# Performance work log

Hardware: AMD Instinct MI355X
Metric: run time of the kernel (lower is better)

Reference implementation:

```python
import jax, jax.numpy as jnp
import numpy as np

COND = 128  # mask = first 128 dims are condition (True); last 128 are transformed


def _mlp(h, W1, b1, W2, b2, W3, b3):
    h = jax.nn.relu(h @ W1 + b1)
    h = jax.nn.relu(h @ W2 + b2)
    return h @ W3 + b3


def setup_inputs() -> dict:
    key = jax.random.key(0)
    ks = jax.random.split(key, 8)
    B, D, H, T = 65536, 256, 512, 128
    s = 0.02  # small init so exp(tanh(s_vals)) is well-behaved
    inp = {
        "x": jax.random.normal(ks[0], (B, D), dtype=jnp.float32),
        "Ws1": jax.random.normal(ks[1], (COND, H), dtype=jnp.float32) * s,
        "bs1": jnp.zeros((H,), jnp.float32),
        "Ws2": jax.random.normal(ks[2], (H, H), dtype=jnp.float32) * s,
        "bs2": jnp.zeros((H,), jnp.float32),
        "Ws3": jax.random.normal(ks[3], (H, T), dtype=jnp.float32) * s,
        "bs3": jnp.zeros((T,), jnp.float32),
        "Wt1": jax.random.normal(ks[4], (COND, H), dtype=jnp.float32) * s,
        "bt1": jnp.zeros((H,), jnp.float32),
        "Wt2": jax.random.normal(ks[5], (H, H), dtype=jnp.float32) * s,
        "bt2": jnp.zeros((H,), jnp.float32),
        "Wt3": jax.random.normal(ks[6], (H, T), dtype=jnp.float32) * s,
        "bt3": jnp.zeros((T,), jnp.float32),
    }
    return inp


def reference(x, Ws1, bs1, Ws2, bs2, Ws3, bs3, Wt1, bt1, Wt2, bt2, Wt3, bt3):
    # mask gather: condition = masked dims, transform = the rest
    cond = x[:, :COND]            # [B, COND]
    x_t = x[:, COND:]             # [B, T]
    s_vals = jnp.tanh(_mlp(cond, Ws1, bs1, Ws2, bs2, Ws3, bs3))  # [B, T]
    t_vals = _mlp(cond, Wt1, bt1, Wt2, bt2, Wt3, bt3)            # [B, T]
    y_partial = x_t * jnp.exp(s_vals) + t_vals                   # forward branch (inverse=False)
    log_det = s_vals.sum(axis=1)                                 # [B]
    y = jnp.concatenate([cond, y_partial], axis=1)               # scatter back
    return (y, log_det)
```

## Files before the change

kernel.cpp:

```cpp
#include <hip/hip_runtime.h>
#include <hip/hip_bf16.h>

typedef __bf16          bf16x8_t __attribute__((ext_vector_type(8)));
typedef float           f32x4_t  __attribute__((ext_vector_type(4)));
typedef unsigned short  u16x4_t  __attribute__((ext_vector_type(4)));

#define DIN      256
#define CONDN    128
#define BM       64
#define NTHREADS 512
#define NWAVE    8

#define OFF_WS1 0
#define OFF_WS2 65536
#define OFF_WS3 327680
#define OFF_WT1 393216
#define OFF_WT2 458752
#define OFF_WT3 720896
#define W_TOTAL 786432

__global__ void prep_w(const float* __restrict__ Ws1, const float* __restrict__ Ws2,
                       const float* __restrict__ Ws3, const float* __restrict__ Wt1,
                       const float* __restrict__ Wt2, const float* __restrict__ Wt3,
                       __hip_bfloat16* __restrict__ wt) {
  int idx = blockIdx.x * blockDim.x + threadIdx.x;
  if (idx >= W_TOTAL) return;
  const float* W; int K, N, off;
  if (idx < OFF_WS2)      { W = Ws1; K = 128; N = 512; off = idx - OFF_WS1; }
  else if (idx < OFF_WS3) { W = Ws2; K = 512; N = 512; off = idx - OFF_WS2; }
  else if (idx < OFF_WT1) { W = Ws3; K = 512; N = 128; off = idx - OFF_WS3; }
  else if (idx < OFF_WT2) { W = Wt1; K = 128; N = 512; off = idx - OFF_WT1; }
  else if (idx < OFF_WT3) { W = Wt2; K = 512; N = 512; off = idx - OFF_WT2; }
  else                    { W = Wt3; K = 512; N = 128; off = idx - OFF_WT3; }
  int n = off / K;
  int k = off - n * K;
  wt[idx] = __float2bfloat16(W[k * N + n]);
}

#define SWZ(row, col) (((((col) >> 3) ^ ((row) & 7)) << 3) + ((col) & 7))

template<int KTOT, int MT, int NT>
__device__ __forceinline__ void mm_tile(const __hip_bfloat16* __restrict__ As, const int lda,
                                        const __hip_bfloat16* __restrict__ Bsrc,
                                        const int l15, const int l4, f32x4_t acc[MT][NT]) {
  const int xr = l15 & 7;
  bf16x8_t a[MT], b[NT], bn[NT];
  #pragma unroll
  for (int n = 0; n < NT; ++n)
    b[n] = *reinterpret_cast<const bf16x8_t*>(&Bsrc[(n * 16 + l15) * KTOT + l4 * 8]);
  #pragma unroll
  for (int kk = 0; kk < KTOT; kk += 32) {
    if (kk + 32 < KTOT) {
      #pragma unroll
      for (int n = 0; n < NT; ++n)
        bn[n] = *reinterpret_cast<const bf16x8_t*>(&Bsrc[(n * 16 + l15) * KTOT + kk + 32 + l4 * 8]);
    }
    #pragma unroll
    for (int m = 0; m < MT; ++m)
      a[m] = *reinterpret_cast<const bf16x8_t*>(
          &As[(m * 16 + l15) * lda + ((((kk >> 3) + l4) ^ xr) << 3)]);
    #pragma unroll
    for (int m = 0; m < MT; ++m) {
      #pragma unroll
      for (int n = 0; n < NT; ++n)
        acc[m][n] = __builtin_amdgcn_mfma_f32_16x16x32_bf16(a[m], b[n], acc[m][n], 0, 0, 0);
    }
    if (kk + 32 < KTOT) {
      #pragma unroll
      for (int n = 0; n < NT; ++n) b[n] = bn[n];
    }
  }
}

template<int MT, int NT, int LD>
__device__ __forceinline__ void relu_store(f32x4_t acc[MT][NT], const float* __restrict__ bias,
                                           const int n0, const int l15, const int l4,
                                           __hip_bfloat16* __restrict__ H) {
  #pragma unroll
  for (int n = 0; n < NT; ++n) {
    const int col = n0 + n * 16 + l15;
    const float bv = bias[col];
    #pragma unroll
    for (int m = 0; m < MT; ++m) {
      #pragma unroll
      for (int r = 0; r < 4; ++r) {
        const int row = m * 16 + l4 * 4 + r;
        float v = fmaxf(acc[m][n][r] + bv, 0.0f);
        H[row * LD + SWZ(row, col)] = __float2bfloat16(v);
      }
    }
  }
}

#define ZERO_ACC(acc, MT, NT) do {                       \
    _Pragma("unroll") for (int m_ = 0; m_ < MT; ++m_)    \
    _Pragma("unroll") for (int n_ = 0; n_ < NT; ++n_)    \
      acc[m_][n_] = (f32x4_t){0.f, 0.f, 0.f, 0.f};       \
  } while (0)

__global__ __launch_bounds__(NTHREADS, 2)
void realnvp_fused(const float* __restrict__ x, const __hip_bfloat16* __restrict__ wt,
                   const float* __restrict__ bs1, const float* __restrict__ bs2,
                   const float* __restrict__ bs3, const float* __restrict__ bt1,
                   const float* __restrict__ bt2, const float* __restrict__ bt3,
                   float* __restrict__ y, float* __restrict__ ld) {
  __shared__ __hip_bfloat16 sA[BM * CONDN];
  __shared__ __hip_bfloat16 sH[BM * 512];
  float* sLd = reinterpret_cast<float*>(sA);

  const int tid  = threadIdx.x;
  const int lane = tid & 63;
  const int wid  = tid >> 6;
  const int l15  = lane & 15;
  const int l4   = lane >> 4;
  const int row0 = blockIdx.x * BM;
  const int n0   = wid * 64;
  const int n3   = wid * 16;

  #pragma unroll
  for (int i = 0; i < 4; ++i) {
    int f = tid + i * NTHREADS;
    int r = f >> 5;
    int c = (f & 31) << 2;
    const float4 v = *reinterpret_cast<const float4*>(&x[(size_t)(row0 + r) * DIN + c]);
    *reinterpret_cast<float4*>(&y[(size_t)(row0 + r) * DIN + c]) = v;
    union { u16x4_t u; __hip_bfloat16 b[4]; } p;
    p.b[0] = __float2bfloat16(v.x); p.b[1] = __float2bfloat16(v.y);
    p.b[2] = __float2bfloat16(v.z); p.b[3] = __float2bfloat16(v.w);
    *reinterpret_cast<u16x4_t*>(&sA[r * CONDN + SWZ(r, c)]) = p.u;
  }
  __syncthreads();

  f32x4_t acc[4][4];
  f32x4_t sfrag[4], tfrag[4];

  ZERO_ACC(acc, 4, 4);
  mm_tile<128, 4, 4>(sA, CONDN, wt + OFF_WS1 + (size_t)n0 * 128, l15, l4, acc);
  relu_store<4, 4, 512>(acc, bs1, n0, l15, l4, sH);
  __syncthreads();
  ZERO_ACC(acc, 4, 4);
  mm_tile<512, 4, 4>(sH, 512, wt + OFF_WS2 + (size_t)n0 * 512, l15, l4, acc);
  __syncthreads();
  relu_store<4, 4, 512>(acc, bs2, n0, l15, l4, sH);
  __syncthreads();
  {
    f32x4_t a3[4][1];
    ZERO_ACC(a3, 4, 1);
    mm_tile<512, 4, 1>(sH, 512, wt + OFF_WS3 + (size_t)n3 * 512, l15, l4, a3);
    #pragma unroll
    for (int m = 0; m < 4; ++m) sfrag[m] = a3[m][0];
  }
  __syncthreads();

  ZERO_ACC(acc, 4, 4);
  mm_tile<128, 4, 4>(sA, CONDN, wt + OFF_WT1 + (size_t)n0 * 128, l15, l4, acc);
  relu_store<4, 4, 512>(acc, bt1, n0, l15, l4, sH);
  __syncthreads();
  ZERO_ACC(acc, 4, 4);
  mm_tile<512, 4, 4>(sH, 512, wt + OFF_WT2 + (size_t)n0 * 512, l15, l4, acc);
  __syncthreads();
  relu_store<4, 4, 512>(acc, bt2, n0, l15, l4, sH);
  __syncthreads();
  {
    f32x4_t a3[4][1];
    ZERO_ACC(a3, 4, 1);
    mm_tile<512, 4, 1>(sH, 512, wt + OFF_WT3 + (size_t)n3 * 512, l15, l4, a3);
    #pragma unroll
    for (int m = 0; m < 4; ++m) tfrag[m] = a3[m][0];
  }

  const float bsv = bs3[n3 + l15];
  const float btv = bt3[n3 + l15];
  #pragma unroll
  for (int m = 0; m < 4; ++m) {
    #pragma unroll
    for (int r = 0; r < 4; ++r) {
      const int rl   = m * 16 + l4 * 4 + r;
      const int grow = row0 + rl;
      const int col  = n3 + l15;
      float s = tanhf(sfrag[m][r] + bsv);
      float t = tfrag[m][r] + btv;
      float xv = x[(size_t)grow * DIN + CONDN + col];
      y[(size_t)grow * DIN + CONDN + col] = xv * expf(s) + t;
      float ss = s;
      ss += __shfl_xor(ss, 1);
      ss += __shfl_xor(ss, 2);
      ss += __shfl_xor(ss, 4);
      ss += __shfl_xor(ss, 8);
      if (l15 == 0) sLd[wid * BM + rl] = ss;
    }
  }
  __syncthreads();
  if (tid < BM) {
    float v = 0.f;
    #pragma unroll
    for (int w = 0; w < NWAVE; ++w) v += sLd[w * BM + tid];
    ld[row0 + tid] = v;
  }
}

extern "C" void kernel_launch(void* const* d_in, const int* in_sizes, int n_in,
                              void* d_out, int out_size, void* d_ws, size_t ws_size,
                              hipStream_t stream) {
  const float* x   = (const float*)d_in[0];
  const float* Ws1 = (const float*)d_in[1];
  const float* bs1 = (const float*)d_in[2];
  const float* Ws2 = (const float*)d_in[3];
  const float* bs2 = (const float*)d_in[4];
  const float* Ws3 = (const float*)d_in[5];
  const float* bs3 = (const float*)d_in[6];
  const float* Wt1 = (const float*)d_in[7];
  const float* bt1 = (const float*)d_in[8];
  const float* Wt2 = (const float*)d_in[9];
  const float* bt2 = (const float*)d_in[10];
  const float* Wt3 = (const float*)d_in[11];
  const float* bt3 = (const float*)d_in[12];

  const int Btot = in_sizes[0] / DIN;
  float* y  = (float*)d_out;
  float* ld = (float*)d_out + (size_t)Btot * DIN;
  __hip_bfloat16* wt = (__hip_bfloat16*)d_ws;

  prep_w<<<(W_TOTAL + 255) / 256, 256, 0, stream>>>(Ws1, Ws2, Ws3, Wt1, Wt2, Wt3, wt);
  realnvp_fused<<<Btot / BM, NTHREADS, 0, stream>>>(x, wt, bs1, bs2, bs3,
                                                    bt1, bt2, bt3, y, ld);
}
```

Measured before the change: 240.4 us.

## Enlarge row tile to 112 rows and add ring-buffered N=1 output GEMM

The per-block row tile grows from 64 to 112 rows (7 MFMA m-tiles per wave), with bounds handling for a ragged last block. Each weight fragment loaded from global/L2 is now reused across more rows. Occupancy drops to one block per SM, since launch bounds and the larger LDS footprint allow only one. A dedicated final-layer GEMM keeps a 4-deep ring of prefetched weight fragments, and the main k-loop is only partially unrolled to limit register pressure.

```diff
diff --git a/kernel.cpp b/kernel.cpp
--- a/kernel.cpp
+++ b/kernel.cpp
@@ -7,7 +7,8 @@
 
 #define DIN      256
 #define CONDN    128
-#define BM       64
+#define BM       112
+#define MT       7
 #define NTHREADS 512
 #define NWAVE    8
 
@@ -39,28 +40,29 @@
 
 #define SWZ(row, col) (((((col) >> 3) ^ ((row) & 7)) << 3) + ((col) & 7))
 
-template<int KTOT, int MT, int NT>
+template<int KTOT, int MTT, int NT>
 __device__ __forceinline__ void mm_tile(const __hip_bfloat16* __restrict__ As, const int lda,
                                         const __hip_bfloat16* __restrict__ Bsrc,
-                                        const int l15, const int l4, f32x4_t acc[MT][NT]) {
+                                        const int l15, const int l4, f32x4_t acc[MTT][NT]) {
   const int xr = l15 & 7;
-  bf16x8_t a[MT], b[NT], bn[NT];
+  const __hip_bfloat16* bp = Bsrc + (size_t)l15 * KTOT + l4 * 8;
+  bf16x8_t a[MTT], b[NT], bn[NT];
   #pragma unroll
   for (int n = 0; n < NT; ++n)
-    b[n] = *reinterpret_cast<const bf16x8_t*>(&Bsrc[(n * 16 + l15) * KTOT + l4 * 8]);
-  #pragma unroll
+    b[n] = *reinterpret_cast<const bf16x8_t*>(bp + n * 16 * KTOT);
+  #pragma unroll 4
   for (int kk = 0; kk < KTOT; kk += 32) {
     if (kk + 32 < KTOT) {
       #pragma unroll
       for (int n = 0; n < NT; ++n)
-        bn[n] = *reinterpret_cast<const bf16x8_t*>(&Bsrc[(n * 16 + l15) * KTOT + kk + 32 + l4 * 8]);
-    }
-    #pragma unroll
-    for (int m = 0; m < MT; ++m)
+        bn[n] = *reinterpret_cast<const bf16x8_t*>(bp + n * 16 * KTOT + kk + 32);
+    }
+    #pragma unroll
+    for (int m = 0; m < MTT; ++m)
       a[m] = *reinterpret_cast<const bf16x8_t*>(
           &As[(m * 16 + l15) * lda + ((((kk >> 3) + l4) ^ xr) << 3)]);
     #pragma unroll
-    for (int m = 0; m < MT; ++m) {
+    for (int m = 0; m < MTT; ++m) {
       #pragma unroll
       for (int n = 0; n < NT; ++n)
         acc[m][n] = __builtin_amdgcn_mfma_f32_16x16x32_bf16(a[m], b[n], acc[m][n], 0, 0, 0);
@@ -72,8 +74,33 @@
   }
 }
 
-template<int MT, int NT, int LD>
-__device__ __forceinline__ void relu_store(f32x4_t acc[MT][NT], const float* __restrict__ bias,
+template<int KTOT, int MTT>
+__device__ __forceinline__ void mm_tile_n1(const __hip_bfloat16* __restrict__ As, const int lda,
+                                           const __hip_bfloat16* __restrict__ Bsrc,
+                                           const int l15, const int l4, f32x4_t acc[MTT]) {
+  const int xr = l15 & 7;
+  const __hip_bfloat16* bp = Bsrc + (size_t)l15 * KTOT + l4 * 8;
+  constexpr int NS = KTOT / 32;
+  bf16x8_t ring[4], a[MTT];
+  #pragma unroll
+  for (int p = 0; p < 4 && p < NS; ++p)
+    ring[p] = *reinterpret_cast<const bf16x8_t*>(bp + p * 32);
+  #pragma unroll
+  for (int s = 0; s < NS; ++s) {
+    #pragma unroll
+    for (int m = 0; m < MTT; ++m)
+      a[m] = *reinterpret_cast<const bf16x8_t*>(
+          &As[(m * 16 + l15) * lda + (((s * 4 + l4) ^ xr) << 3)]);
+    #pragma unroll
+    for (int m = 0; m < MTT; ++m)
+      acc[m] = __builtin_amdgcn_mfma_f32_16x16x32_bf16(a[m], ring[s & 3], acc[m], 0, 0, 0);
+    if (s + 4 < NS)
+      ring[s & 3] = *reinterpret_cast<const bf16x8_t*>(bp + (s + 4) * 32);
+  }
+}
+
+template<int MTT, int NT, int LD>
+__device__ __forceinline__ void relu_store(f32x4_t acc[MTT][NT], const float* __restrict__ bias,
                                            const int n0, const int l15, const int l4,
                                            __hip_bfloat16* __restrict__ H) {
   #pragma unroll
@@ -81,7 +108,7 @@
     const int col = n0 + n * 16 + l15;
     const float bv = bias[col];
     #pragma unroll
-    for (int m = 0; m < MT; ++m) {
+    for (int m = 0; m < MTT; ++m) {
       #pragma unroll
       for (int r = 0; r < 4; ++r) {
         const int row = m * 16 + l4 * 4 + r;
@@ -92,18 +119,18 @@
   }
 }
 
-#define ZERO_ACC(acc, MT, NT) do {                       \
-    _Pragma("unroll") for (int m_ = 0; m_ < MT; ++m_)    \
-    _Pragma("unroll") for (int n_ = 0; n_ < NT; ++n_)    \
-      acc[m_][n_] = (f32x4_t){0.f, 0.f, 0.f, 0.f};       \
+#define ZERO_ACC(acc, MTT, NT) do {                       \
+    _Pragma("unroll") for (int m_ = 0; m_ < MTT; ++m_)    \
+    _Pragma("unroll") for (int n_ = 0; n_ < NT; ++n_)     \
+      acc[m_][n_] = (f32x4_t){0.f, 0.f, 0.f, 0.f};        \
   } while (0)
 
-__global__ __launch_bounds__(NTHREADS, 2)
+__global__ __launch_bounds__(NTHREADS, 1)
 void realnvp_fused(const float* __restrict__ x, const __hip_bfloat16* __restrict__ wt,
                    const float* __restrict__ bs1, const float* __restrict__ bs2,
                    const float* __restrict__ bs3, const float* __restrict__ bt1,
                    const float* __restrict__ bt2, const float* __restrict__ bt3,
-                   float* __restrict__ y, float* __restrict__ ld) {
+                   float* __restrict__ y, float* __restrict__ ld, const int Btot) {
   __shared__ __hip_bfloat16 sA[BM * CONDN];
   __shared__ __hip_bfloat16 sH[BM * 512];
   float* sLd = reinterpret_cast<float*>(sA);
@@ -114,74 +141,83 @@
   const int l15  = lane & 15;
   const int l4   = lane >> 4;
   const int row0 = blockIdx.x * BM;
+  const int V    = min(BM, Btot - row0);
   const int n0   = wid * 64;
   const int n3   = wid * 16;
 
   #pragma unroll
-  for (int i = 0; i < 4; ++i) {
+  for (int i = 0; i < 7; ++i) {
     int f = tid + i * NTHREADS;
     int r = f >> 5;
     int c = (f & 31) << 2;
-    const float4 v = *reinterpret_cast<const float4*>(&x[(size_t)(row0 + r) * DIN + c]);
-    *reinterpret_cast<float4*>(&y[(size_t)(row0 + r) * DIN + c]) = v;
-    union { u16x4_t u; __hip_bfloat16 b[4]; } p;
-    p.b[0] = __float2bfloat16(v.x); p.b[1] = __float2bfloat16(v.y);
-    p.b[2] = __float2bfloat16(v.z); p.b[3] = __float2bfloat16(v.w);
-    *reinterpret_cast<u16x4_t*>(&sA[r * CONDN + SWZ(r, c)]) = p.u;
-  }
-  __syncthreads();
-
-  f32x4_t acc[4][4];
-  f32x4_t sfrag[4], tfrag[4];
-
-  ZERO_ACC(acc, 4, 4);
-  mm_tile<128, 4, 4>(sA, CONDN, wt + OFF_WS1 + (size_t)n0 * 128, l15, l4, acc);
-  relu_store<4, 4, 512>(acc, bs1, n0, l15, l4, sH);
-  __syncthreads();
-  ZERO_ACC(acc, 4, 4);
-  mm_tile<512, 4, 4>(sH, 512, wt + OFF_WS2 + (size_t)n0 * 512, l15, l4, acc);
-  __syncthreads();
-  relu_store<4, 4, 512>(acc, bs2, n0, l15, l4, sH);
+    if (r < V) {
+      const float4 v = *reinterpret_cast<const float4*>(&x[(size_t)(row0 + r) * DIN + c]);
+      *reinterpret_cast<float4*>(&y[(size_t)(row0 + r) * DIN + c]) = v;
+      union { u16x4_t u; __hip_bfloat16 b[4]; } p;
+      p.b[0] = __float2bfloat16(v.x); p.b[1] = __float2bfloat16(v.y);
+      p.b[2] = __float2bfloat16(v.z); p.b[3] = __float2bfloat16(v.w);
+      *reinterpret_cast<u16x4_t*>(&sA[r * CONDN + SWZ(r, c)]) = p.u;
+    } else {
+      *reinterpret_cast<u16x4_t*>(&sA[r * CONDN + SWZ(r, c)]) = (u16x4_t){0, 0, 0, 0};
+    }
+  }
+  __syncthreads();
+
+  f32x4_t acc[MT][4];
+  f32x4_t sfrag[MT], tfrag[MT];
+
+  ZERO_ACC(acc, MT, 4);
+  mm_tile<128, MT, 4>(sA, CONDN, wt + OFF_WS1 + (size_t)n0 * 128, l15, l4, acc);
+  relu_store<MT, 4, 512>(acc, bs1, n0, l15, l4, sH);
+  __syncthreads();
+  ZERO_ACC(acc, MT, 4);
+  mm_tile<512, MT, 4>(sH, 512, wt + OFF_WS2 + (size_t)n0 * 512, l15, l4, acc);
+  __syncthreads();
+  relu_store<MT, 4, 512>(acc, bs2, n0, l15, l4, sH);
   __syncthreads();
   {
-    f32x4_t a3[4][1];
-    ZERO_ACC(a3, 4, 1);
-    mm_tile<512, 4, 1>(sH, 512, wt + OFF_WS3 + (size_t)n3 * 512, l15, l4, a3);
-    #pragma unroll
-    for (int m = 0; m < 4; ++m) sfrag[m] = a3[m][0];
-  }
-  __syncthreads();
-
-  ZERO_ACC(acc, 4, 4);
-  mm_tile<128, 4, 4>(sA, CONDN, wt + OFF_WT1 + (size_t)n0 * 128, l15, l4, acc);
-  relu_store<4, 4, 512>(acc, bt1, n0, l15, l4, sH);
-  __syncthreads();
-  ZERO_ACC(acc, 4, 4);
-  mm_tile<512, 4, 4>(sH, 512, wt + OFF_WT2 + (size_t)n0 * 512, l15, l4, acc);
-  __syncthreads();
-  relu_store<4, 4, 512>(acc, bt2, n0, l15, l4, sH);
+    f32x4_t a3[MT];
+    #pragma unroll
+    for (int m = 0; m < MT; ++m) a3[m] = (f32x4_t){0.f, 0.f, 0.f, 0.f};
+    mm_tile_n1<512, MT>(sH, 512, wt + OFF_WS3 + (size_t)n3 * 512, l15, l4, a3);
+    #pragma unroll
+    for (int m = 0; m < MT; ++m) sfrag[m] = a3[m];
+  }
+  __syncthreads();
+
+  ZERO_ACC(acc, MT, 4);
+  mm_tile<128, MT, 4>(sA, CONDN, wt + OFF_WT1 + (size_t)n0 * 128, l15, l4, acc);
+  relu_store<MT, 4, 512>(acc, bt1, n0, l15, l4, sH);
+  __syncthreads();
+  ZERO_ACC(acc, MT, 4);
+  mm_tile<512, MT, 4>(sH, 512, wt + OFF_WT2 + (size_t)n0 * 512, l15, l4, acc);
+  __syncthreads();
+  relu_store<MT, 4, 512>(acc, bt2, n0, l15, l4, sH);
   __syncthreads();
   {
-    f32x4_t a3[4][1];
-    ZERO_ACC(a3, 4, 1);
-    mm_tile<512, 4, 1>(sH, 512, wt + OFF_WT3 + (size_t)n3 * 512, l15, l4, a3);
-    #pragma unroll
-    for (int m = 0; m < 4; ++m) tfrag[m] = a3[m][0];
+    f32x4_t a3[MT];
+    #pragma unroll
+    for (int m = 0; m < MT; ++m) a3[m] = (f32x4_t){0.f, 0.f, 0.f, 0.f};
+    mm_tile_n1<512, MT>(sH, 512, wt + OFF_WT3 + (size_t)n3 * 512, l15, l4, a3);
+    #pragma unroll
+    for (int m = 0; m < MT; ++m) tfrag[m] = a3[m];
   }
 
   const float bsv = bs3[n3 + l15];
   const float btv = bt3[n3 + l15];
   #pragma unroll
-  for (int m = 0; m < 4; ++m) {
+  for (int m = 0; m < MT; ++m) {
     #pragma unroll
     for (int r = 0; r < 4; ++r) {
       const int rl   = m * 16 + l4 * 4 + r;
       const int grow = row0 + rl;
       const int col  = n3 + l15;
       float s = tanhf(sfrag[m][r] + bsv);
-      float t = tfrag[m][r] + btv;
-      float xv = x[(size_t)grow * DIN + CONDN + col];
-      y[(size_t)grow * DIN + CONDN + col] = xv * expf(s) + t;
+      if (grow < Btot) {
+        float t  = tfrag[m][r] + btv;
+        float xv = x[(size_t)grow * DIN + CONDN + col];
+        y[(size_t)grow * DIN + CONDN + col] = xv * expf(s) + t;
+      }
       float ss = s;
       ss += __shfl_xor(ss, 1);
       ss += __shfl_xor(ss, 2);
@@ -191,7 +227,7 @@
     }
   }
   __syncthreads();
-  if (tid < BM) {
+  if (tid < BM && row0 + tid < Btot) {
     float v = 0.f;
     #pragma unroll
     for (int w = 0; w < NWAVE; ++w) v += sLd[w * BM + tid];
@@ -222,6 +258,7 @@
   __hip_bfloat16* wt = (__hip_bfloat16*)d_ws;
 
   prep_w<<<(W_TOTAL + 255) / 256, 256, 0, stream>>>(Ws1, Ws2, Ws3, Wt1, Wt2, Wt3, wt);
-  realnvp_fused<<<Btot / BM, NTHREADS, 0, stream>>>(x, wt, bs1, bs2, bs3,
-                                                    bt1, bt2, bt3, y, ld);
-}
+  const int grid = (Btot + BM - 1) / BM;
+  realnvp_fused<<<grid, NTHREADS, 0, stream>>>(x, wt, bs1, bs2, bs3,
+                                               bt1, bt2, bt3, y, ld, Btot);
+}
```

Result: slower. 431.3 us (+79.4%).

## Use 16 waves per block with split-K final layer and deeper B prefetch ring

Applied to the files above, without the earlier changes.

Doubles the block to 1024 threads (16 waves), so each wave computes 32 hidden columns instead of 64. The final 512→128 layers are split along K across two wave groups, with partial sums combined through new LDS buffers. The B-operand register prefetch becomes a 3-deep ring. The aim is more latency hiding and less per-wave register pressure, at the cost of more LDS, an extra barrier, occupancy limited to one block per CU, and half the waves idling in the epilogue.

```diff
diff --git a/kernel.cpp b/kernel.cpp
--- a/kernel.cpp
+++ b/kernel.cpp
@@ -8,8 +8,9 @@
 #define DIN      256
 #define CONDN    128
 #define BM       64
-#define NTHREADS 512
-#define NWAVE    8
+#define NTHREADS 1024
+#define NWAVE    16
+#define LDS_S    132
 
 #define OFF_WS1 0
 #define OFF_WS2 65536
@@ -39,41 +40,44 @@
 
 #define SWZ(row, col) (((((col) >> 3) ^ ((row) & 7)) << 3) + ((col) & 7))
 
-template<int KTOT, int MT, int NT>
+template<int KTOT, int LDB, int MTT, int NT>
 __device__ __forceinline__ void mm_tile(const __hip_bfloat16* __restrict__ As, const int lda,
                                         const __hip_bfloat16* __restrict__ Bsrc,
-                                        const int l15, const int l4, f32x4_t acc[MT][NT]) {
+                                        const int l15, const int l4, f32x4_t acc[MTT][NT]) {
   const int xr = l15 & 7;
-  bf16x8_t a[MT], b[NT], bn[NT];
-  #pragma unroll
-  for (int n = 0; n < NT; ++n)
-    b[n] = *reinterpret_cast<const bf16x8_t*>(&Bsrc[(n * 16 + l15) * KTOT + l4 * 8]);
-  #pragma unroll
-  for (int kk = 0; kk < KTOT; kk += 32) {
-    if (kk + 32 < KTOT) {
+  const __hip_bfloat16* bp = Bsrc + (size_t)l15 * LDB + l4 * 8;
+  constexpr int NS = KTOT / 32;
+  constexpr int DEPTH = (NS < 3) ? NS : 3;
+  bf16x8_t ring[DEPTH][NT];
+  bf16x8_t a[MTT];
+  #pragma unroll
+  for (int p = 0; p < DEPTH; ++p) {
+    #pragma unroll
+    for (int n = 0; n < NT; ++n)
+      ring[p][n] = *reinterpret_cast<const bf16x8_t*>(bp + (size_t)n * 16 * LDB + p * 32);
+  }
+  #pragma unroll
+  for (int s = 0; s < NS; ++s) {
+    #pragma unroll
+    for (int m = 0; m < MTT; ++m)
+      a[m] = *reinterpret_cast<const bf16x8_t*>(
+          &As[(m * 16 + l15) * lda + (((s * 4 + l4) ^ xr) << 3)]);
+    #pragma unroll
+    for (int m = 0; m < MTT; ++m) {
       #pragma unroll
       for (int n = 0; n < NT; ++n)
-        bn[n] = *reinterpret_cast<const bf16x8_t*>(&Bsrc[(n * 16 + l15) * KTOT + kk + 32 + l4 * 8]);
-    }
-    #pragma unroll
-    for (int m = 0; m < MT; ++m)
-      a[m] = *reinterpret_cast<const bf16x8_t*>(
-          &As[(m * 16 + l15) * lda + ((((kk >> 3) + l4) ^ xr) << 3)]);
-    #pragma unroll
-    for (int m = 0; m < MT; ++m) {
+        acc[m][n] = __builtin_amdgcn_mfma_f32_16x16x32_bf16(a[m], ring[s % DEPTH][n], acc[m][n], 0, 0, 0);
+    }
+    if (s + DEPTH < NS) {
       #pragma unroll
       for (int n = 0; n < NT; ++n)
-        acc[m][n] = __builtin_amdgcn_mfma_f32_16x16x32_bf16(a[m], b[n], acc[m][n], 0, 0, 0);
-    }
-    if (kk + 32 < KTOT) {
-      #pragma unroll
-      for (int n = 0; n < NT; ++n) b[n] = bn[n];
-    }
-  }
-}
-
-template<int MT, int NT, int LD>
-__device__ __forceinline__ void relu_store(f32x4_t acc[MT][NT], const float* __restrict__ bias,
+        ring[s % DEPTH][n] = *reinterpret_cast<const bf16x8_t*>(bp + (size_t)n * 16 * LDB + (s + DEPTH) * 32);
+    }
+  }
+}
+
+template<int MTT, int NT, int LD>
+__device__ __forceinline__ void relu_store(f32x4_t acc[MTT][NT], const float* __restrict__ bias,
                                            const int n0, const int l15, const int l4,
                                            __hip_bfloat16* __restrict__ H) {
   #pragma unroll
@@ -81,7 +85,7 @@
     const int col = n0 + n * 16 + l15;
     const float bv = bias[col];
     #pragma unroll
-    for (int m = 0; m < MT; ++m) {
+    for (int m = 0; m < MTT; ++m) {
       #pragma unroll
       for (int r = 0; r < 4; ++r) {
         const int row = m * 16 + l4 * 4 + r;
@@ -92,13 +96,13 @@
   }
 }
 
-#define ZERO_ACC(acc, MT, NT) do {                       \
-    _Pragma("unroll") for (int m_ = 0; m_ < MT; ++m_)    \
-    _Pragma("unroll") for (int n_ = 0; n_ < NT; ++n_)    \
-      acc[m_][n_] = (f32x4_t){0.f, 0.f, 0.f, 0.f};       \
+#define ZERO_ACC(acc, MTT, NT) do {                       \
+    _Pragma("unroll") for (int m_ = 0; m_ < MTT; ++m_)    \
+    _Pragma("unroll") for (int n_ = 0; n_ < NT; ++n_)     \
+      acc[m_][n_] = (f32x4_t){0.f, 0.f, 0.f, 0.f};        \
   } while (0)
 
-__global__ __launch_bounds__(NTHREADS, 2)
+__global__ __launch_bounds__(NTHREADS, 1)
 void realnvp_fused(const float* __restrict__ x, const __hip_bfloat16* __restrict__ wt,
                    const float* __restrict__ bs1, const float* __restrict__ bs2,
                    const float* __restrict__ bs3, const float* __restrict__ bt1,
@@ -106,6 +110,8 @@
                    float* __restrict__ y, float* __restrict__ ld) {
   __shared__ __hip_bfloat16 sA[BM * CONDN];
   __shared__ __hip_bfloat16 sH[BM * 512];
+  __shared__ float sS[BM * LDS_S];
+  __shared__ float tS[BM * LDS_S];
   float* sLd = reinterpret_cast<float*>(sA);
 
   const int tid  = threadIdx.x;
@@ -114,11 +120,13 @@
   const int l15  = lane & 15;
   const int l4   = lane >> 4;
   const int row0 = blockIdx.x * BM;
-  const int n0   = wid * 64;
-  const int n3   = wid * 16;
-
-  #pragma unroll
-  for (int i = 0; i < 4; ++i) {
+  const int n0   = wid * 32;
+  const int g    = wid >> 3;
+  const int wA   = wid & 7;
+  const int n3   = wA * 16;
+
+  #pragma unroll
+  for (int i = 0; i < 2; ++i) {
     int f = tid + i * NTHREADS;
     int r = f >> 5;
     int c = (f & 31) << 2;
@@ -131,70 +139,91 @@
   }
   __syncthreads();
 
-  f32x4_t acc[4][4];
+  f32x4_t acc[4][2];
   f32x4_t sfrag[4], tfrag[4];
 
-  ZERO_ACC(acc, 4, 4);
-  mm_tile<128, 4, 4>(sA, CONDN, wt + OFF_WS1 + (size_t)n0 * 128, l15, l4, acc);
-  relu_store<4, 4, 512>(acc, bs1, n0, l15, l4, sH);
-  __syncthreads();
-  ZERO_ACC(acc, 4, 4);
-  mm_tile<512, 4, 4>(sH, 512, wt + OFF_WS2 + (size_t)n0 * 512, l15, l4, acc);
-  __syncthreads();
-  relu_store<4, 4, 512>(acc, bs2, n0, l15, l4, sH);
+  ZERO_ACC(acc, 4, 2);
+  mm_tile<128, 128, 4, 2>(sA, CONDN, wt + OFF_WS1 + (size_t)n0 * 128, l15, l4, acc);
+  relu_store<4, 2, 512>(acc, bs1, n0, l15, l4, sH);
+  __syncthreads();
+  ZERO_ACC(acc, 4, 2);
+  mm_tile<512, 512, 4, 2>(sH, 512, wt + OFF_WS2 + (size_t)n0 * 512, l15, l4, acc);
+  __syncthreads();
+  relu_store<4, 2, 512>(acc, bs2, n0, l15, l4, sH);
   __syncthreads();
   {
     f32x4_t a3[4][1];
     ZERO_ACC(a3, 4, 1);
-    mm_tile<512, 4, 1>(sH, 512, wt + OFF_WS3 + (size_t)n3 * 512, l15, l4, a3);
-    #pragma unroll
-    for (int m = 0; m < 4; ++m) sfrag[m] = a3[m][0];
-  }
-  __syncthreads();
-
-  ZERO_ACC(acc, 4, 4);
-  mm_tile<128, 4, 4>(sA, CONDN, wt + OFF_WT1 + (size_t)n0 * 128, l15, l4, acc);
-  relu_store<4, 4, 512>(acc, bt1, n0, l15, l4, sH);
-  __syncthreads();
-  ZERO_ACC(acc, 4, 4);
-  mm_tile<512, 4, 4>(sH, 512, wt + OFF_WT2 + (size_t)n0 * 512, l15, l4, acc);
-  __syncthreads();
-  relu_store<4, 4, 512>(acc, bt2, n0, l15, l4, sH);
+    mm_tile<256, 512, 4, 1>(sH + g * 256, 512,
+                            wt + OFF_WS3 + (size_t)n3 * 512 + g * 256, l15, l4, a3);
+    if (g == 0) {
+      #pragma unroll
+      for (int m = 0; m < 4; ++m) sfrag[m] = a3[m][0];
+    } else {
+      #pragma unroll
+      for (int m = 0; m < 4; ++m)
+        #pragma unroll
+        for (int r = 0; r < 4; ++r)
+          sS[(m * 16 + l4 * 4 + r) * LDS_S + n3 + l15] = a3[m][0][r];
+    }
+  }
+  __syncthreads();
+
+  ZERO_ACC(acc, 4, 2);
+  mm_tile<128, 128, 4, 2>(sA, CONDN, wt + OFF_WT1 + (size_t)n0 * 128, l15, l4, acc);
+  relu_store<4, 2, 512>(acc, bt1, n0, l15, l4, sH);
+  __syncthreads();
+  ZERO_ACC(acc, 4, 2);
+  mm_tile<512, 512, 4, 2>(sH, 512, wt + OFF_WT2 + (size_t)n0 * 512, l15, l4, acc);
+  __syncthreads();
+  relu_store<4, 2, 512>(acc, bt2, n0, l15, l4, sH);
   __syncthreads();
   {
     f32x4_t a3[4][1];
     ZERO_ACC(a3, 4, 1);
-    mm_tile<512, 4, 1>(sH, 512, wt + OFF_WT3 + (size_t)n3 * 512, l15, l4, a3);
-    #pragma unroll
-    for (int m = 0; m < 4; ++m) tfrag[m] = a3[m][0];
-  }
-
-  const float bsv = bs3[n3 + l15];
-  const float btv = bt3[n3 + l15];
-  #pragma unroll
-  for (int m = 0; m < 4; ++m) {
-    #pragma unroll
-    for (int r = 0; r < 4; ++r) {
-      const int rl   = m * 16 + l4 * 4 + r;
-      const int grow = row0 + rl;
-      const int col  = n3 + l15;
-      float s = tanhf(sfrag[m][r] + bsv);
-      float t = tfrag[m][r] + btv;
-      float xv = x[(size_t)grow * DIN + CONDN + col];
-      y[(size_t)grow * DIN + CONDN + col] = xv * expf(s) + t;
-      float ss = s;
-      ss += __shfl_xor(ss, 1);
-      ss += __shfl_xor(ss, 2);
-      ss += __shfl_xor(ss, 4);
-      ss += __shfl_xor(ss, 8);
-      if (l15 == 0) sLd[wid * BM + rl] = ss;
+    mm_tile<256, 512, 4, 1>(sH + g * 256, 512,
+                            wt + OFF_WT3 + (size_t)n3 * 512 + g * 256, l15, l4, a3);
+    if (g == 0) {
+      #pragma unroll
+      for (int m = 0; m < 4; ++m) tfrag[m] = a3[m][0];
+    } else {
+      #pragma unroll
+      for (int m = 0; m < 4; ++m)
+        #pragma unroll
+        for (int r = 0; r < 4; ++r)
+          tS[(m * 16 + l4 * 4 + r) * LDS_S + n3 + l15] = a3[m][0][r];
+    }
+  }
+  __syncthreads();
+
+  if (g == 0) {
+    const float bsv = bs3[n3 + l15];
+    const float btv = bt3[n3 + l15];
+    #pragma unroll
+    for (int m = 0; m < 4; ++m) {
+      #pragma unroll
+      for (int r = 0; r < 4; ++r) {
+        const int rl   = m * 16 + l4 * 4 + r;
+        const int grow = row0 + rl;
+        const int col  = n3 + l15;
+        float s = tanhf(sfrag[m][r] + sS[rl * LDS_S + col] + bsv);
+        float t = tfrag[m][r] + tS[rl * LDS_S + col] + btv;
+        float xv = x[(size_t)grow * DIN + CONDN + col];
+        y[(size_t)grow * DIN + CONDN + col] = xv * expf(s) + t;
+        float ss = s;
+        ss += __shfl_xor(ss, 1);
+        ss += __shfl_xor(ss, 2);
+        ss += __shfl_xor(ss, 4);
+        ss += __shfl_xor(ss, 8);
+        if (l15 == 0) sLd[wA * BM + rl] = ss;
+      }
     }
   }
   __syncthreads();
   if (tid < BM) {
     float v = 0.f;
     #pragma unroll
-    for (int w = 0; w < NWAVE; ++w) v += sLd[w * BM + tid];
+    for (int w = 0; w < 8; ++w) v += sLd[w * BM + tid];
     ld[row0 + tid] = v;
   }
 }
```

Measured after the change: 271.8 us. 1.13x slower.

## Stage weight tiles into LDS with double-buffered async global_load_lds pipeline

Applied to the files above, without the earlier changes.

Re-layouts the bf16 weights into 32-wide K tiles and streams each tile into a double-buffered LDS region with global_load_lds, prefetching the next tile (including the next layer's first tile) while MFMAs run on the current one. Each wave now reads its B fragments from LDS instead of from global memory, so the whole block shares one fetch of each weight tile. The cost is an extra 64KB of LDS and a block barrier per K step. Launch bounds drop to one block per SM-pair setting, which lowers occupancy.

```diff
diff --git a/kernel.cpp b/kernel.cpp
--- a/kernel.cpp
+++ b/kernel.cpp
@@ -10,6 +10,7 @@
 #define BM       64
 #define NTHREADS 512
 #define NWAVE    8
+#define BUFE     16384
 
 #define OFF_WS1 0
 #define OFF_WS2 65536
@@ -25,55 +26,87 @@
                        __hip_bfloat16* __restrict__ wt) {
   int idx = blockIdx.x * blockDim.x + threadIdx.x;
   if (idx >= W_TOTAL) return;
-  const float* W; int K, N, off;
-  if (idx < OFF_WS2)      { W = Ws1; K = 128; N = 512; off = idx - OFF_WS1; }
-  else if (idx < OFF_WS3) { W = Ws2; K = 512; N = 512; off = idx - OFF_WS2; }
-  else if (idx < OFF_WT1) { W = Ws3; K = 512; N = 128; off = idx - OFF_WS3; }
-  else if (idx < OFF_WT2) { W = Wt1; K = 128; N = 512; off = idx - OFF_WT1; }
-  else if (idx < OFF_WT3) { W = Wt2; K = 512; N = 512; off = idx - OFF_WT2; }
-  else                    { W = Wt3; K = 512; N = 128; off = idx - OFF_WT3; }
-  int n = off / K;
-  int k = off - n * K;
-  wt[idx] = __float2bfloat16(W[k * N + n]);
+  const float* W; int lgN, off;
+  if (idx < OFF_WS2)      { W = Ws1; lgN = 9; off = OFF_WS1; }
+  else if (idx < OFF_WS3) { W = Ws2; lgN = 9; off = OFF_WS2; }
+  else if (idx < OFF_WT1) { W = Ws3; lgN = 7; off = OFF_WS3; }
+  else if (idx < OFF_WT2) { W = Wt1; lgN = 9; off = OFF_WT1; }
+  else if (idx < OFF_WT3) { W = Wt2; lgN = 9; off = OFF_WT2; }
+  else                    { W = Wt3; lgN = 7; off = OFF_WT3; }
+  const int e    = idx - off;
+  const int lgT  = lgN + 5;
+  const int tile = e >> lgT;
+  const int rem  = e & ((1 << lgT) - 1);
+  const int c    = rem >> 3;
+  const int j    = rem & 7;
+  const int o    = c >> lgN;
+  const int n    = c & ((1 << lgN) - 1);
+  const int k    = tile * 32 + o * 8 + j;
+  wt[idx] = __float2bfloat16(W[(k << lgN) + n]);
 }
 
 #define SWZ(row, col) (((((col) >> 3) ^ ((row) & 7)) << 3) + ((col) & 7))
 
-template<int KTOT, int MT, int NT>
-__device__ __forceinline__ void mm_tile(const __hip_bfloat16* __restrict__ As, const int lda,
-                                        const __hip_bfloat16* __restrict__ Bsrc,
-                                        const int l15, const int l4, f32x4_t acc[MT][NT]) {
+template<int NTILE>
+__device__ __forceinline__ void stage_w(__hip_bfloat16* __restrict__ dstbuf,
+                                        const __hip_bfloat16* __restrict__ src0,
+                                        const int wid, const int lane) {
+  constexpr int ROUNDS = (NTILE * 4) / 512;
+  #pragma unroll
+  for (int r = 0; r < ROUNDS; ++r) {
+    const int cbase = (r * 8 + wid) * 64;
+    const __hip_bfloat16* src = src0 + (size_t)(cbase + lane) * 8;
+    __hip_bfloat16* dst = dstbuf + (size_t)cbase * 8;
+    __builtin_amdgcn_global_load_lds(
+        (const __attribute__((address_space(1))) void*)src,
+        (__attribute__((address_space(3))) void*)dst, 16, 0, 0);
+  }
+}
+
+template<int NS, int NTILE, int MTT, int NT, class NextFn>
+__device__ __forceinline__ void gemm_layer(
+    const __hip_bfloat16* __restrict__ As, const int lda,
+    const __hip_bfloat16* __restrict__ wseg, __hip_bfloat16* __restrict__ sW,
+    unsigned& tc, const int wid, const int lane, const int l15, const int l4,
+    const int n0, f32x4_t acc[MTT][NT], NextFn next_stage)
+{
   const int xr = l15 & 7;
-  bf16x8_t a[MT], b[NT], bn[NT];
-  #pragma unroll
-  for (int n = 0; n < NT; ++n)
-    b[n] = *reinterpret_cast<const bf16x8_t*>(&Bsrc[(n * 16 + l15) * KTOT + l4 * 8]);
-  #pragma unroll
-  for (int kk = 0; kk < KTOT; kk += 32) {
-    if (kk + 32 < KTOT) {
-      #pragma unroll
-      for (int n = 0; n < NT; ++n)
-        bn[n] = *reinterpret_cast<const bf16x8_t*>(&Bsrc[(n * 16 + l15) * KTOT + kk + 32 + l4 * 8]);
-    }
-    #pragma unroll
-    for (int m = 0; m < MT; ++m)
-      a[m] = *reinterpret_cast<const bf16x8_t*>(
-          &As[(m * 16 + l15) * lda + ((((kk >> 3) + l4) ^ xr) << 3)]);
-    #pragma unroll
-    for (int m = 0; m < MT; ++m) {
+  bf16x8_t a[MTT], an[MTT], b[NT];
+  #pragma unroll
+  for (int m = 0; m < MTT; ++m)
+    a[m] = *reinterpret_cast<const bf16x8_t*>(&As[(m * 16 + l15) * lda + ((l4 ^ xr) << 3)]);
+  #pragma unroll 1
+  for (int s = 0; s < NS; ++s) {
+    __hip_bfloat16* nbuf = sW + ((tc + 1) & 1) * BUFE;
+    if (s + 1 < NS) stage_w<NTILE>(nbuf, wseg + (size_t)(s + 1) * (NTILE * 32), wid, lane);
+    else            next_stage(nbuf);
+    const __hip_bfloat16* cbuf = sW + (tc & 1) * BUFE;
+    #pragma unroll
+    for (int n = 0; n < NT; ++n)
+      b[n] = *reinterpret_cast<const bf16x8_t*>(&cbuf[(size_t)(l4 * NTILE + n0 + n * 16 + l15) * 8]);
+    if (s + 1 < NS) {
+      #pragma unroll
+      for (int m = 0; m < MTT; ++m)
+        an[m] = *reinterpret_cast<const bf16x8_t*>(
+            &As[(m * 16 + l15) * lda + ((((s + 1) * 4 + l4) ^ xr) << 3)]);
+    }
+    #pragma unroll
+    for (int m = 0; m < MTT; ++m) {
       #pragma unroll
       for (int n = 0; n < NT; ++n)
         acc[m][n] = __builtin_amdgcn_mfma_f32_16x16x32_bf16(a[m], b[n], acc[m][n], 0, 0, 0);
     }
-    if (kk + 32 < KTOT) {
-      #pragma unroll
-      for (int n = 0; n < NT; ++n) b[n] = bn[n];
-    }
-  }
-}
-
-template<int MT, int NT, int LD>
-__device__ __forceinline__ void relu_store(f32x4_t acc[MT][NT], const float* __restrict__ bias,
+    if (s + 1 < NS) {
+      #pragma unroll
+      for (int m = 0; m < MTT; ++m) a[m] = an[m];
+    }
+    ++tc;
+    __syncthreads();
+  }
+}
+
+template<int MTT, int NT, int LD>
+__device__ __forceinline__ void relu_store(f32x4_t acc[MTT][NT], const float* __restrict__ bias,
                                            const int n0, const int l15, const int l4,
                                            __hip_bfloat16* __restrict__ H) {
   #pragma unroll
@@ -81,7 +114,7 @@
     const int col = n0 + n * 16 + l15;
     const float bv = bias[col];
     #pragma unroll
-    for (int m = 0; m < MT; ++m) {
+    for (int m = 0; m < MTT; ++m) {
       #pragma unroll
       for (int r = 0; r < 4; ++r) {
         const int row = m * 16 + l4 * 4 + r;
@@ -92,13 +125,13 @@
   }
 }
 
-#define ZERO_ACC(acc, MT, NT) do {                       \
-    _Pragma("unroll") for (int m_ = 0; m_ < MT; ++m_)    \
-    _Pragma("unroll") for (int n_ = 0; n_ < NT; ++n_)    \
-      acc[m_][n_] = (f32x4_t){0.f, 0.f, 0.f, 0.f};       \
+#define ZERO_ACC(acc, MTT, NT) do {                       \
+    _Pragma("unroll") for (int m_ = 0; m_ < MTT; ++m_)    \
+    _Pragma("unroll") for (int n_ = 0; n_ < NT; ++n_)     \
+      acc[m_][n_] = (f32x4_t){0.f, 0.f, 0.f, 0.f};        \
   } while (0)
 
-__global__ __launch_bounds__(NTHREADS, 2)
+__global__ __launch_bounds__(NTHREADS, 1)
 void realnvp_fused(const float* __restrict__ x, const __hip_bfloat16* __restrict__ wt,
                    const float* __restrict__ bs1, const float* __restrict__ bs2,
                    const float* __restrict__ bs3, const float* __restrict__ bt1,
@@ -106,6 +139,7 @@
                    float* __restrict__ y, float* __restrict__ ld) {
   __shared__ __hip_bfloat16 sA[BM * CONDN];
   __shared__ __hip_bfloat16 sH[BM * 512];
+  __shared__ __hip_bfloat16 sW[2 * BUFE];
   float* sLd = reinterpret_cast<float*>(sA);
 
   const int tid  = threadIdx.x;
@@ -114,8 +148,10 @@
   const int l15  = lane & 15;
   const int l4   = lane >> 4;
   const int row0 = blockIdx.x * BM;
-  const int n0   = wid * 64;
+  const int n064 = wid * 64;
   const int n3   = wid * 16;
+
+  stage_w<512>(sW, wt + OFF_WS1, wid, lane);
 
   #pragma unroll
   for (int i = 0; i < 4; ++i) {
@@ -131,40 +167,48 @@
   }
   __syncthreads();
 
+  unsigned tc = 0;
   f32x4_t acc[4][4];
   f32x4_t sfrag[4], tfrag[4];
 
   ZERO_ACC(acc, 4, 4);
-  mm_tile<128, 4, 4>(sA, CONDN, wt + OFF_WS1 + (size_t)n0 * 128, l15, l4, acc);
-  relu_store<4, 4, 512>(acc, bs1, n0, l15, l4, sH);
-  __syncthreads();
-  ZERO_ACC(acc, 4, 4);
-  mm_tile<512, 4, 4>(sH, 512, wt + OFF_WS2 + (size_t)n0 * 512, l15, l4, acc);
-  __syncthreads();
-  relu_store<4, 4, 512>(acc, bs2, n0, l15, l4, sH);
-  __syncthreads();
+  gemm_layer<4, 512, 4, 4>(sA, CONDN, wt + OFF_WS1, sW, tc, wid, lane, l15, l4, n064, acc,
+      [&](__hip_bfloat16* nbuf) { stage_w<512>(nbuf, wt + OFF_WS2, wid, lane); });
+  relu_store<4, 4, 512>(acc, bs1, n064, l15, l4, sH);
+  __syncthreads();
+
+  ZERO_ACC(acc, 4, 4);
+  gemm_layer<16, 512, 4, 4>(sH, 512, wt + OFF_WS2, sW, tc, wid, lane, l15, l4, n064, acc,
+      [&](__hip_bfloat16* nbuf) { stage_w<128>(nbuf, wt + OFF_WS3, wid, lane); });
+  relu_store<4, 4, 512>(acc, bs2, n064, l15, l4, sH);
+  __syncthreads();
+
   {
     f32x4_t a3[4][1];
     ZERO_ACC(a3, 4, 1);
-    mm_tile<512, 4, 1>(sH, 512, wt + OFF_WS3 + (size_t)n3 * 512, l15, l4, a3);
+    gemm_layer<16, 128, 4, 1>(sH, 512, wt + OFF_WS3, sW, tc, wid, lane, l15, l4, n3, a3,
+        [&](__hip_bfloat16* nbuf) { stage_w<512>(nbuf, wt + OFF_WT1, wid, lane); });
     #pragma unroll
     for (int m = 0; m < 4; ++m) sfrag[m] = a3[m][0];
   }
-  __syncthreads();
-
-  ZERO_ACC(acc, 4, 4);
-  mm_tile<128, 4, 4>(sA, CONDN, wt + OFF_WT1 + (size_t)n0 * 128, l15, l4, acc);
-  relu_store<4, 4, 512>(acc, bt1, n0, l15, l4, sH);
-  __syncthreads();
-  ZERO_ACC(acc, 4, 4);
-  mm_tile<512, 4, 4>(sH, 512, wt + OFF_WT2 + (size_t)n0 * 512, l15, l4, acc);
-  __syncthreads();
-  relu_store<4, 4, 512>(acc, bt2, n0, l15, l4, sH);
-  __syncthreads();
+
+  ZERO_ACC(acc, 4, 4);
+  gemm_layer<4, 512, 4, 4>(sA, CONDN, wt + OFF_WT1, sW, tc, wid, lane, l15, l4, n064, acc,
+      [&](__hip_bfloat16* nbuf) { stage_w<512>(nbuf, wt + OFF_WT2, wid, lane); });
+  relu_store<4, 4, 512>(acc, bt1, n064, l15, l4, sH);
+  __syncthreads();
+
+  ZERO_ACC(acc, 4, 4);
+  gemm_layer<16, 512, 4, 4>(sH, 512, wt + OFF_WT2, sW, tc, wid, lane, l15, l4, n064, acc,
+      [&](__hip_bfloat16* nbuf) { stage_w<128>(nbuf, wt + OFF_WT3, wid, lane); });
+  relu_store<4, 4, 512>(acc, bt2, n064, l15, l4, sH);
+  __syncthreads();
+
   {
     f32x4_t a3[4][1];
     ZERO_ACC(a3, 4, 1);
-    mm_tile<512, 4, 1>(sH, 512, wt + OFF_WT3 + (size_t)n3 * 512, l15, l4, a3);
+    gemm_layer<16, 128, 4, 1>(sH, 512, wt + OFF_WT3, sW, tc, wid, lane, l15, l4, n3, a3,
+        [&](__hip_bfloat16*) {});
     #pragma unroll
     for (int m = 0; m < 4; ++m) tfrag[m] = a3[m][0];
   }
```

New measurement: 244.3 us. No clear change (+1.6%).
